# Kernel optimization log

Measured on AMD Instinct MI355X. Metric: run time of the kernel, lower is better.

## Reference

```python
import jax, jax.numpy as jnp
import numpy as np

N_HEADS = 16
ROPE_BASE = 10000.0

def rotate_half(x):
    x1, x2 = jnp.split(x, 2, axis=-1)
    return jnp.concatenate([-x2, x1], axis=-1)

def rope_tables(T, D, dtype):
    inv_freq = 1.0 / (ROPE_BASE ** (np.arange(0, D, 2, dtype=np.float32) / D))
    t = np.arange(T, dtype=np.float32)
    freqs = np.outer(t, inv_freq)            # [T, D/2]
    emb = np.concatenate([freqs, freqs], -1)  # [T, D]
    return jnp.asarray(np.cos(emb), dtype), jnp.asarray(np.sin(emb), dtype)

def setup_inputs() -> dict:
    key = jax.random.key(0)
    ks = jax.random.split(key, 5)
    B, T, C, D = 2, 2048, 1024, 64
    s = 0.02
    return {
        "x":  jax.random.normal(ks[0], (B, T, C), jnp.float32),
        "Wq": jax.random.normal(ks[1], (C, C), jnp.float32) * s,
        "Wk": jax.random.normal(ks[2], (C, D), jnp.float32) * s,
        "Wv": jax.random.normal(ks[3], (C, D), jnp.float32) * s,
        "Wo": jax.random.normal(ks[4], (C, C), jnp.float32) * s,
    }

def reference(x, Wq, Wk, Wv, Wo):
    B, T, C = x.shape
    H = N_HEADS
    D = C // H
    scale = D ** -0.5
    q = (x @ Wq).reshape(B, T, H, D).transpose(0, 2, 1, 3)  # [B,H,T,D]
    k = x @ Wk                                              # [B,T,D] single KV head
    v = x @ Wv                                              # [B,T,D]
    cos, sin = rope_tables(T, D, x.dtype)                   # [T,D]
    q = q * cos + rotate_half(q) * sin                      # broadcast over B,H
    k = k * cos + rotate_half(k) * sin                      # broadcast over B
    # MQA causal attention: shared K/V head broadcast to all query heads
    scores = jnp.einsum('bhqd,bkd->bhqk', q, k) * scale     # [B,H,T,T]
    causal = jnp.tril(jnp.ones((T, T), bool))
    scores = jnp.where(causal, scores, jnp.finfo(scores.dtype).min)
    attn = jax.nn.softmax(scores, axis=-1)
    out = jnp.einsum('bhqk,bkd->bhqd', attn, v)             # [B,H,T,D]
    out = out.transpose(0, 2, 1, 3).reshape(B, T, C)
    return out @ Wo
```

## Files before the change

kernel.cpp:

```cpp
#include <hip/hip_runtime.h>
#include <hip/hip_bf16.h>

typedef _Float16 f16;
typedef __attribute__((ext_vector_type(8))) _Float16 f16x8;
typedef __attribute__((ext_vector_type(4))) _Float16 f16x4;
typedef __attribute__((ext_vector_type(4))) float f32x4;

#define MFMA16(a, b, c) __builtin_amdgcn_mfma_f32_16x16x32_f16(a, b, c, 0, 0, 0)

__device__ __forceinline__ void gload_lds16(const void* g, void* l)
{
    __builtin_amdgcn_global_load_lds(
        (const __attribute__((address_space(1))) unsigned int*)g,
        (__attribute__((address_space(3))) unsigned int*)l, 16, 0, 0);
}

__global__ __launch_bounds__(256) void cvt_all_kernel(const float* __restrict__ x, const float* __restrict__ Wq,
                                                      const float* __restrict__ Wk, const float* __restrict__ Wv,
                                                      const float* __restrict__ Wo, f16* __restrict__ xb,
                                                      f16* __restrict__ WallT, f16* __restrict__ WoT)
{
    int i = blockIdx.x * 256 + threadIdx.x;
    if (i < 1048576) {
        float4 v = ((const float4*)x)[i];
        f16x4 o;
        o[0] = (f16)v.x; o[1] = (f16)v.y; o[2] = (f16)v.z; o[3] = (f16)v.w;
        *(f16x4*)(xb + 4 * (size_t)i) = o;
        return;
    }
    const float* src;
    f16* dstbase;
    int n4, k4, ldN;
    if (i < 1114112) {
        int j = i - 1048576;
        n4 = (j & 255) * 4; k4 = (j >> 8) * 4;
        src = Wq; ldN = 1024; dstbase = WallT + (size_t)n4 * 1024;
    } else if (i < 1122304) {
        int j = i - 1114112;
        int p4 = (j & 31) * 4; k4 = (j >> 5) * 4;
        if (p4 < 64) {
            n4 = (p4 >= 16 && p4 < 48) ? (p4 ^ 48) : p4;
            src = Wk;
        } else {
            n4 = p4 - 64;
            src = Wv;
        }
        ldN = 64; dstbase = WallT + (size_t)(1024 + p4) * 1024;
    } else {
        int j = i - 1122304;
        n4 = (j & 255) * 4; k4 = (j >> 8) * 4;
        src = Wo; ldN = 1024; dstbase = WoT + (size_t)n4 * 1024;
    }
    float4 v0 = *(const float4*)(src + (size_t)(k4 + 0) * ldN + n4);
    float4 v1 = *(const float4*)(src + (size_t)(k4 + 1) * ldN + n4);
    float4 v2 = *(const float4*)(src + (size_t)(k4 + 2) * ldN + n4);
    float4 v3 = *(const float4*)(src + (size_t)(k4 + 3) * ldN + n4);
    float a0[4] = {v0.x, v0.y, v0.z, v0.w};
    float a1[4] = {v1.x, v1.y, v1.z, v1.w};
    float a2[4] = {v2.x, v2.y, v2.z, v2.w};
    float a3[4] = {v3.x, v3.y, v3.z, v3.w};
#pragma unroll
    for (int jj = 0; jj < 4; ++jj) {
        f16x4 o;
        o[0] = (f16)a0[jj]; o[1] = (f16)a1[jj]; o[2] = (f16)a2[jj]; o[3] = (f16)a3[jj];
        *(f16x4*)(dstbase + (size_t)jj * 1024 + k4) = o;
    }
}

template<int MODE>
__global__ __launch_bounds__(256) void gemm_bt(const f16* __restrict__ A, const f16* __restrict__ Bt,
                                               void* __restrict__ Cv, f16* __restrict__ kout, f16* __restrict__ vout,
                                               int NBX)
{
    __shared__ __align__(16) f16 As[128 * 64];
    __shared__ __align__(16) f16 Bs[64 * 64];
    int id = blockIdx.x;
    int qn = gridDim.x >> 3;
    int lin = (id & 7) * qn + (id >> 3);
    int bx = lin % NBX, by = lin / NBX;
    int tid = threadIdx.x, lane = tid & 63, wid = tid >> 6;
    int wr = wid >> 1, wc = wid & 1;
    int lrow = lane & 15, gq = lane >> 4;
    f32x4 acc[4][2];
#pragma unroll
    for (int fm = 0; fm < 4; ++fm)
#pragma unroll
        for (int fn = 0; fn < 2; ++fn) acc[fm][fn] = (f32x4){0.f, 0.f, 0.f, 0.f};

    for (int kt = 0; kt < 16; ++kt) {
        int k0 = kt * 64;
#pragma unroll
        for (int i = 0; i < 4; ++i) {
            int c = wid * 4 + i;
            int row = c * 8 + (lane >> 3);
            int slot = (lane & 7) ^ (row & 7);
            gload_lds16(A + (size_t)(by * 128 + row) * 1024 + k0 + slot * 8, &As[c * 512 + lane * 8]);
        }
#pragma unroll
        for (int i = 0; i < 2; ++i) {
            int c = wid * 2 + i;
            int row = c * 8 + (lane >> 3);
            int slot = (lane & 7) ^ (row & 7);
            gload_lds16(Bt + (size_t)(bx * 64 + row) * 1024 + k0 + slot * 8, &Bs[c * 512 + lane * 8]);
        }
        __syncthreads();
#pragma unroll
        for (int ks = 0; ks < 2; ++ks) {
            f16x8 af[4], bf[2];
#pragma unroll
            for (int fm = 0; fm < 4; ++fm) {
                int row = wr * 64 + fm * 16 + lrow;
                int slot = (ks * 4 + gq) ^ (row & 7);
                af[fm] = *(const f16x8*)&As[row * 64 + slot * 8];
            }
#pragma unroll
            for (int fn = 0; fn < 2; ++fn) {
                int row = wc * 32 + fn * 16 + lrow;
                int slot = (ks * 4 + gq) ^ (row & 7);
                bf[fn] = *(const f16x8*)&Bs[row * 64 + slot * 8];
            }
#pragma unroll
            for (int fm = 0; fm < 4; ++fm)
#pragma unroll
                for (int fn = 0; fn < 2; ++fn)
                    acc[fm][fn] = MFMA16(af[fm], bf[fn], acc[fm][fn]);
        }
        __syncthreads();
    }
    if constexpr (MODE == 1) {
        float* C = (float*)Cv;
#pragma unroll
        for (int fm = 0; fm < 4; ++fm)
#pragma unroll
            for (int fn = 0; fn < 2; ++fn)
#pragma unroll
                for (int r = 0; r < 4; ++r) {
                    int row = by * 128 + wr * 64 + fm * 16 + gq * 4 + r;
                    int col = bx * 64 + wc * 32 + fn * 16 + lrow;
                    C[(size_t)row * 1024 + col] = acc[fm][fn][r];
                }
    } else {
        if (bx < 16) {
            f16* C = (f16*)Cv;
#pragma unroll
            for (int fm = 0; fm < 4; ++fm)
#pragma unroll
                for (int fn = 0; fn < 2; ++fn)
#pragma unroll
                    for (int r = 0; r < 4; ++r) {
                        int row = by * 128 + wr * 64 + fm * 16 + gq * 4 + r;
                        int col = bx * 64 + wc * 32 + fn * 16 + lrow;
                        C[(size_t)row * 1024 + col] = (f16)acc[fm][fn][r];
                    }
        } else if (bx == 16) {
            const float L2B = 13.287712379549449f / 64.0f;
            int i = wc * 16 + lrow;
            float invf = exp2f(-(float)(2 * i) * L2B);
#pragma unroll
            for (int fm = 0; fm < 4; ++fm)
#pragma unroll
                for (int r = 0; r < 4; ++r) {
                    int row = by * 128 + wr * 64 + fm * 16 + gq * 4 + r;
                    float t = (float)(row & 2047);
                    float ss, cc;
                    sincosf(t * invf, &ss, &cc);
                    float x1 = acc[fm][0][r], x2 = acc[fm][1][r];
                    kout[(size_t)row * 64 + i]      = (f16)(x1 * cc - x2 * ss);
                    kout[(size_t)row * 64 + i + 32] = (f16)(x2 * cc + x1 * ss);
                }
        } else {
#pragma unroll
            for (int fm = 0; fm < 4; ++fm)
#pragma unroll
                for (int fn = 0; fn < 2; ++fn) {
                    int d = wc * 32 + fn * 16 + lrow;
                    int rowbase = by * 128 + wr * 64 + fm * 16 + gq * 4;
                    f16x4 pw;
#pragma unroll
                    for (int r = 0; r < 4; ++r) pw[r] = (f16)acc[fm][fn][r];
                    *(f16x4*)&vout[(size_t)d * 4096 + rowbase] = pw;
                }
        }
    }
}

#define SOFTMAX(S, MM, LL, OO, PSF) do {                                            \
    float mx = fmaxf(fmaxf(fmaxf(S[0][0],S[0][1]),fmaxf(S[0][2],S[0][3])),          \
                     fmaxf(fmaxf(S[1][0],S[1][1]),fmaxf(S[1][2],S[1][3])));         \
    mx = fmaxf(mx, fmaxf(fmaxf(fmaxf(S[2][0],S[2][1]),fmaxf(S[2][2],S[2][3])),      \
                         fmaxf(fmaxf(S[3][0],S[3][1]),fmaxf(S[3][2],S[3][3]))));    \
    mx = fmaxf(mx, __shfl_xor(mx, 16));                                             \
    mx = fmaxf(mx, __shfl_xor(mx, 32));                                             \
    if (!__all(mx <= MM + 3.0f)) {                                                  \
        float mn = fmaxf(MM, mx);                                                   \
        float alpha = exp2f(MM - mn);                                               \
        MM = mn; LL *= alpha;                                                       \
        float av0 = __shfl(alpha, g * 4 + 0), av1 = __shfl(alpha, g * 4 + 1);       \
        float av2 = __shfl(alpha, g * 4 + 2), av3 = __shfl(alpha, g * 4 + 3);       \
        _Pragma("unroll")                                                           \
        for (int dt = 0; dt < 4; ++dt) {                                            \
            OO[dt][0] *= av0; OO[dt][1] *= av1; OO[dt][2] *= av2; OO[dt][3] *= av3; \
        }                                                                           \
    }                                                                               \
    float rs = 0.f;                                                                 \
    _Pragma("unroll")                                                               \
    for (int tt = 0; tt < 4; ++tt) {                                                \
        f16x4 pw;                                                                   \
        _Pragma("unroll")                                                           \
        for (int r = 0; r < 4; ++r) {                                               \
            float pp = exp2f(S[tt][r] - MM); S[tt][r] = pp; pw[r] = (f16)pp;        \
        }                                                                           \
        rs += (S[tt][0] + S[tt][1]) + (S[tt][2] + S[tt][3]);                        \
        *(f16x4*)&PSF[lrow * 64 + ((tt * 16 + g * 4) ^ swl)] = pw;                  \
    }                                                                               \
    LL += rs;                                                                       \
} while (0)

__global__ __launch_bounds__(256, 3) void attn_kernel(const f16* __restrict__ q, const f16* __restrict__ k,
                                                      const f16* __restrict__ vt, f16* __restrict__ ao,
                                                      char* __restrict__ partial)
{
    constexpr int T = 2048;
    int c = blockIdx.x, y = blockIdx.y;
    int b = y >> 3, hA = y & 7, hB = hA + 8;
    int qt, ch;
    if (c < 16)      { qt = 16 + c; ch = 0; }
    else if (c < 32) { qt = c;      ch = 1; }
    else             { qt = 47 - c; ch = 0; }
    int nt = qt + 1;
    int nch = (qt >= 16) ? 2 : 1;
    int tbeg = ch * 16;
    int tend = min(nt, tbeg + 16);

    int tid = threadIdx.x, lane = tid & 63, wid = tid >> 6;
    int lrow = lane & 15, g = lane >> 4;
    int qw = qt * 64 + wid * 16;
    int swl = (lrow & 7) << 3;

    __shared__ __align__(16) f16 Ks[2][64 * 64];
    __shared__ __align__(16) f16 Vs[2][64 * 64];
    __shared__ __align__(16) f16 PsM[4][2][16 * 64];

    const f16* qrowA = q + (size_t)(b * T + qw + lrow) * 1024 + hA * 64;
    const f16* qrowB = qrowA + (hB - hA) * 64;
    f16x8 xA0 = *(const f16x8*)&qrowA[g * 8];
    f16x8 xA1 = *(const f16x8*)&qrowA[g * 8 + 32];
    f16x8 xB0 = *(const f16x8*)&qrowB[g * 8];
    f16x8 xB1 = *(const f16x8*)&qrowB[g * 8 + 32];
    f16x8 qfA0, qfA1, qfB0, qfB1;
    {
        const float qsc = 0.125f * 1.4426950408889634f;
        const float L2B = 13.287712379549449f / 64.0f;
        float t_ = (float)(qw + lrow);
#pragma unroll
        for (int j = 0; j < 8; ++j) {
            int i = g * 8 + j;
            float invf = exp2f(-(float)(2 * i) * L2B);
            float ss, cc;
            sincosf(t_ * invf, &ss, &cc);
            float a0 = (float)xA0[j], a1 = (float)xA1[j];
            qfA0[j] = (f16)((a0 * cc - a1 * ss) * qsc);
            qfA1[j] = (f16)((a1 * cc + a0 * ss) * qsc);
            float b0 = (float)xB0[j], b1 = (float)xB1[j];
            qfB0[j] = (f16)((b0 * cc - b1 * ss) * qsc);
            qfB1[j] = (f16)((b1 * cc + b0 * ss) * qsc);
        }
    }

    float mA = -1e30f, lA = 0.f, mB = -1e30f, lB = 0.f;
    f32x4 oA[4], oB[4];
#pragma unroll
    for (int dt = 0; dt < 4; ++dt) { oA[dt] = (f32x4){0.f,0.f,0.f,0.f}; oB[dt] = (f32x4){0.f,0.f,0.f,0.f}; }

    const f16* kbase = k + (size_t)b * T * 64;
    const f16* vtbase = vt + (size_t)b * T;

    int srow_lo = lane >> 3, sslot = lane & 7;
#define STAGE(buf, t) do {                                                                   \
    _Pragma("unroll")                                                                        \
    for (int i_ = 0; i_ < 2; ++i_) {                                                         \
        int c2 = wid * 2 + i_;                                                               \
        int row = c2 * 8 + srow_lo;                                                          \
        int slot = sslot ^ (row & 7);                                                        \
        gload_lds16(kbase + (size_t)((t) * 64 + row) * 64 + slot * 8,                        \
                    &Ks[buf][c2 * 512 + lane * 8]);                                          \
        gload_lds16(vtbase + (size_t)row * 4096 + (t) * 64 + slot * 8,                       \
                    &Vs[buf][c2 * 512 + lane * 8]);                                          \
    }                                                                                        \
} while (0)

    STAGE(0, tbeg);
    __syncthreads();
    int cur = 0;

    for (int t = tbeg; t < tend; ++t) {
        if (t + 1 < tend) STAGE(cur ^ 1, t + 1);
        f16* PsA = &PsM[wid][0][0];
        f16* PsBf = &PsM[wid][1][0];
        const f16* Kc = &Ks[cur][0];
        const f16* Vc = &Vs[cur][0];

        f32x4 sA[4], sB[4];
        __builtin_amdgcn_s_setprio(1);
#pragma unroll
        for (int tt = 0; tt < 4; ++tt) {
            f16x8 kf0 = *(const f16x8*)&Kc[(tt * 16 + lrow) * 64 + ((g * 8) ^ swl)];
            f16x8 kf1 = *(const f16x8*)&Kc[(tt * 16 + lrow) * 64 + ((32 + g * 8) ^ swl)];
            f32x4 z = (f32x4){0.f, 0.f, 0.f, 0.f};
            z = MFMA16(kf0, qfA0, z);
            z = MFMA16(kf1, qfA1, z);
            sA[tt] = z;
            z = (f32x4){0.f, 0.f, 0.f, 0.f};
            z = MFMA16(kf0, qfB0, z);
            z = MFMA16(kf1, qfB1, z);
            sB[tt] = z;
        }
        __builtin_amdgcn_s_setprio(0);
        if (t == nt - 1) {
            int qab = qw + lrow;
            int kb0 = t * 64 + g * 4;
#pragma unroll
            for (int tt = 0; tt < 4; ++tt)
#pragma unroll
                for (int r = 0; r < 4; ++r)
                    if (kb0 + tt * 16 + r > qab) { sA[tt][r] = -1e30f; sB[tt][r] = -1e30f; }
        }
        SOFTMAX(sA, mA, lA, oA, PsA);
        SOFTMAX(sB, mB, lB, oB, PsBf);
        __builtin_amdgcn_s_setprio(1);
#pragma unroll
        for (int chk = 0; chk < 2; ++chk) {
            f16x8 pfA = *(const f16x8*)&PsA[lrow * 64 + ((chk * 32 + g * 8) ^ swl)];
            f16x8 pfB = *(const f16x8*)&PsBf[lrow * 64 + ((chk * 32 + g * 8) ^ swl)];
#pragma unroll
            for (int dt = 0; dt < 4; ++dt) {
                f16x8 vf = *(const f16x8*)&Vc[(dt * 16 + lrow) * 64 + ((chk * 32 + g * 8) ^ swl)];
                oA[dt] = MFMA16(pfA, vf, oA[dt]);
                oB[dt] = MFMA16(pfB, vf, oB[dt]);
            }
        }
        __builtin_amdgcn_s_setprio(0);
        __syncthreads();
        cur ^= 1;
    }
#undef STAGE
    lA += __shfl_xor(lA, 16); lA += __shfl_xor(lA, 32);
    lB += __shfl_xor(lB, 16); lB += __shfl_xor(lB, 32);

    if (nch == 1) {
#pragma unroll
        for (int rr = 0; rr < 4; ++rr) {
            float invA = 1.f / __shfl(lA, g * 4 + rr);
            float invB = 1.f / __shfl(lB, g * 4 + rr);
            int qab = qw + g * 4 + rr;
            size_t rowoff = (size_t)(b * T + qab) * 1024;
#pragma unroll
            for (int dt = 0; dt < 4; ++dt) {
                ao[rowoff + hA * 64 + dt * 16 + lrow] = (f16)(oA[dt][rr] * invA);
                ao[rowoff + hB * 64 + dt * 16 + lrow] = (f16)(oB[dt][rr] * invB);
            }
        }
    } else {
        int bhA = b * 16 + hA, bhB = b * 16 + hB;
        char* slotA = partial + ((size_t)(bhA * 16 + (qt - 16)) * 2 + ch) * 8704;
        char* slotB = partial + ((size_t)(bhB * 16 + (qt - 16)) * 2 + ch) * 8704;
        f16* opA = (f16*)slotA; float* mpA = (float*)(slotA + 8192); float* lpA = mpA + 64;
        f16* opB = (f16*)slotB; float* mpB = (float*)(slotB + 8192); float* lpB = mpB + 64;
#pragma unroll
        for (int rr = 0; rr < 4; ++rr) {
            int row = wid * 16 + g * 4 + rr;
#pragma unroll
            for (int dt = 0; dt < 4; ++dt) {
                opA[row * 64 + dt * 16 + lrow] = (f16)oA[dt][rr];
                opB[row * 64 + dt * 16 + lrow] = (f16)oB[dt][rr];
            }
        }
        if (g == 0) {
            mpA[wid * 16 + lrow] = mA; lpA[wid * 16 + lrow] = lA;
            mpB[wid * 16 + lrow] = mB; lpB[wid * 16 + lrow] = lB;
        }
    }
}

__global__ __launch_bounds__(256) void combine_kernel(const char* __restrict__ partial, f16* __restrict__ ao)
{
    constexpr int T = 2048;
    int qt = 16 + blockIdx.x, bh = blockIdx.y;
    int b = bh >> 4, h = bh & 15;
    int tid = threadIdx.x;
    int row = tid >> 2, dp = (tid & 3) * 16;
    const char* s0 = partial + ((size_t)(bh * 16 + (qt - 16)) * 2) * 8704;
    const char* s1 = s0 + 8704;
    const f16* o0 = (const f16*)s0; const float* m0 = (const float*)(s0 + 8192); const float* l0 = m0 + 64;
    const f16* o1 = (const f16*)s1; const float* m1 = (const float*)(s1 + 8192); const float* l1 = m1 + 64;
    float mm0 = m0[row], mm1 = m1[row];
    float M = fmaxf(mm0, mm1);
    float a0 = exp2f(mm0 - M), a1 = exp2f(mm1 - M);
    float inv = 1.f / (l0[row] * a0 + l1[row] * a1);
    f16x8 u0 = ((const f16x8*)(o0 + row * 64 + dp))[0];
    f16x8 u1 = ((const f16x8*)(o0 + row * 64 + dp))[1];
    f16x8 w0 = ((const f16x8*)(o1 + row * 64 + dp))[0];
    f16x8 w1 = ((const f16x8*)(o1 + row * 64 + dp))[1];
    f16x8 r0, r1;
#pragma unroll
    for (int j = 0; j < 8; ++j) {
        r0[j] = (f16)(((float)u0[j] * a0 + (float)w0[j] * a1) * inv);
        r1[j] = (f16)(((float)u1[j] * a0 + (float)w1[j] * a1) * inv);
    }
    f16* dst = ao + (size_t)(b * T + qt * 64 + row) * 1024 + h * 64 + dp;
    *(f16x8*)dst = r0;
    *(f16x8*)(dst + 8) = r1;
}

extern "C" void kernel_launch(void* const* d_in, const int* in_sizes, int n_in,
                              void* d_out, int out_size, void* d_ws, size_t ws_size,
                              hipStream_t stream)
{
    (void)in_sizes; (void)n_in; (void)out_size; (void)ws_size;
    const float* x  = (const float*)d_in[0];
    const float* Wq = (const float*)d_in[1];
    const float* Wk = (const float*)d_in[2];
    const float* Wv = (const float*)d_in[3];
    const float* Wo = (const float*)d_in[4];
    float* out = (float*)d_out;

    char* w = (char*)d_ws;
    size_t off = 0;
    auto alloc = [&](size_t bytes) -> void* {
        void* p = (void*)(w + off);
        off += (bytes + 255) & ~(size_t)255;
        return p;
    };
    f16* xb    = (f16*)alloc(4194304ull * 2);
    f16* WallT = (f16*)alloc(1179648ull * 2);
    f16* WoT   = (f16*)alloc(1048576ull * 2);
    f16* qg    = (f16*)alloc(4194304ull * 2);
    f16* krp   = (f16*)alloc(262144ull * 2);
    f16* vt    = (f16*)alloc(262144ull * 2);
    f16* ao    = (f16*)alloc(4194304ull * 2);
    char* partial = (char*)xb;

    cvt_all_kernel<<<4640, 256, 0, stream>>>(x, Wq, Wk, Wv, Wo, xb, WallT, WoT);
    gemm_bt<0><<<576, 256, 0, stream>>>(xb, WallT, qg, krp, vt, 18);
    attn_kernel<<<dim3(48, 16), 256, 0, stream>>>(qg, krp, vt, ao, partial);
    combine_kernel<<<dim3(16, 32), 256, 0, stream>>>(partial, ao);
    gemm_bt<1><<<512, 256, 0, stream>>>(ao, WoT, out, nullptr, nullptr, 16);
}
```

Measured before the change: 100.2 us.

## Rebalance causal attention split-KV chunks and serialize per-head softmax to cut LDS

The attention work split changes from fixed 16-tile chunks to even splits: query tiles 0-15 use one chunk, 16-25 use two and 26-31 use three. The grid grows to 54 blocks per row, and the combine kernel now merges up to three partials using the new slot layout. The two heads' softmax and PV MFMA phases now share one P scratch buffer in sequence. This halves that LDS footprint so launch bounds can ask for 4 blocks per CU. The softmax also skips the cross-lane max shuffles unless a rescale is needed; the tradeoffs are more partial traffic and less overlap between the two heads.

```diff
diff --git a/kernel.cpp b/kernel.cpp
--- a/kernel.cpp
+++ b/kernel.cpp
@@ -185,13 +185,13 @@
 }
 
 #define SOFTMAX(S, MM, LL, OO, PSF) do {                                            \
-    float mx = fmaxf(fmaxf(fmaxf(S[0][0],S[0][1]),fmaxf(S[0][2],S[0][3])),          \
-                     fmaxf(fmaxf(S[1][0],S[1][1]),fmaxf(S[1][2],S[1][3])));         \
-    mx = fmaxf(mx, fmaxf(fmaxf(fmaxf(S[2][0],S[2][1]),fmaxf(S[2][2],S[2][3])),      \
-                         fmaxf(fmaxf(S[3][0],S[3][1]),fmaxf(S[3][2],S[3][3]))));    \
-    mx = fmaxf(mx, __shfl_xor(mx, 16));                                             \
-    mx = fmaxf(mx, __shfl_xor(mx, 32));                                             \
-    if (!__all(mx <= MM + 3.0f)) {                                                  \
+    float mxl = fmaxf(fmaxf(fmaxf(S[0][0],S[0][1]),fmaxf(S[0][2],S[0][3])),         \
+                      fmaxf(fmaxf(S[1][0],S[1][1]),fmaxf(S[1][2],S[1][3])));        \
+    mxl = fmaxf(mxl, fmaxf(fmaxf(fmaxf(S[2][0],S[2][1]),fmaxf(S[2][2],S[2][3])),    \
+                           fmaxf(fmaxf(S[3][0],S[3][1]),fmaxf(S[3][2],S[3][3]))));  \
+    if (!__all(mxl <= MM + 3.0f)) {                                                 \
+        float mx = fmaxf(mxl, __shfl_xor(mxl, 16));                                 \
+        mx = fmaxf(mx, __shfl_xor(mx, 32));                                         \
         float mn = fmaxf(MM, mx);                                                   \
         float alpha = exp2f(MM - mn);                                               \
         MM = mn; LL *= alpha;                                                       \
@@ -216,21 +216,20 @@
     LL += rs;                                                                       \
 } while (0)
 
-__global__ __launch_bounds__(256, 3) void attn_kernel(const f16* __restrict__ q, const f16* __restrict__ k,
+__global__ __launch_bounds__(256, 4) void attn_kernel(const f16* __restrict__ q, const f16* __restrict__ k,
                                                       const f16* __restrict__ vt, f16* __restrict__ ao,
                                                       char* __restrict__ partial)
 {
     constexpr int T = 2048;
     int c = blockIdx.x, y = blockIdx.y;
     int b = y >> 3, hA = y & 7, hB = hA + 8;
-    int qt, ch;
-    if (c < 16)      { qt = 16 + c; ch = 0; }
-    else if (c < 32) { qt = c;      ch = 1; }
-    else             { qt = 47 - c; ch = 0; }
+    int qt, ch, nch;
+    if (c < 16)      { qt = c; ch = 0; nch = 1; }
+    else if (c < 36) { int j = c - 16; qt = 16 + (j >> 1); ch = j & 1;  nch = 2; }
+    else             { int j = c - 36; qt = 26 + j / 3;    ch = j % 3;  nch = 3; }
     int nt = qt + 1;
-    int nch = (qt >= 16) ? 2 : 1;
-    int tbeg = ch * 16;
-    int tend = min(nt, tbeg + 16);
+    int tbeg = ch * nt / nch;
+    int tend = (ch + 1) * nt / nch;
 
     int tid = threadIdx.x, lane = tid & 63, wid = tid >> 6;
     int lrow = lane & 15, g = lane >> 4;
@@ -239,7 +238,7 @@
 
     __shared__ __align__(16) f16 Ks[2][64 * 64];
     __shared__ __align__(16) f16 Vs[2][64 * 64];
-    __shared__ __align__(16) f16 PsM[4][2][16 * 64];
+    __shared__ __align__(16) f16 PsM[4][16 * 64];
 
     const f16* qrowA = q + (size_t)(b * T + qw + lrow) * 1024 + hA * 64;
     const f16* qrowB = qrowA + (hB - hA) * 64;
@@ -295,8 +294,7 @@
 
     for (int t = tbeg; t < tend; ++t) {
         if (t + 1 < tend) STAGE(cur ^ 1, t + 1);
-        f16* PsA = &PsM[wid][0][0];
-        f16* PsBf = &PsM[wid][1][0];
+        f16* Ps = &PsM[wid][0];
         const f16* Kc = &Ks[cur][0];
         const f16* Vc = &Vs[cur][0];
 
@@ -325,18 +323,27 @@
                 for (int r = 0; r < 4; ++r)
                     if (kb0 + tt * 16 + r > qab) { sA[tt][r] = -1e30f; sB[tt][r] = -1e30f; }
         }
-        SOFTMAX(sA, mA, lA, oA, PsA);
-        SOFTMAX(sB, mB, lB, oB, PsBf);
+        SOFTMAX(sA, mA, lA, oA, Ps);
         __builtin_amdgcn_s_setprio(1);
 #pragma unroll
         for (int chk = 0; chk < 2; ++chk) {
-            f16x8 pfA = *(const f16x8*)&PsA[lrow * 64 + ((chk * 32 + g * 8) ^ swl)];
-            f16x8 pfB = *(const f16x8*)&PsBf[lrow * 64 + ((chk * 32 + g * 8) ^ swl)];
+            f16x8 pf = *(const f16x8*)&Ps[lrow * 64 + ((chk * 32 + g * 8) ^ swl)];
 #pragma unroll
             for (int dt = 0; dt < 4; ++dt) {
                 f16x8 vf = *(const f16x8*)&Vc[(dt * 16 + lrow) * 64 + ((chk * 32 + g * 8) ^ swl)];
-                oA[dt] = MFMA16(pfA, vf, oA[dt]);
-                oB[dt] = MFMA16(pfB, vf, oB[dt]);
+                oA[dt] = MFMA16(pf, vf, oA[dt]);
+            }
+        }
+        __builtin_amdgcn_s_setprio(0);
+        SOFTMAX(sB, mB, lB, oB, Ps);
+        __builtin_amdgcn_s_setprio(1);
+#pragma unroll
+        for (int chk = 0; chk < 2; ++chk) {
+            f16x8 pf = *(const f16x8*)&Ps[lrow * 64 + ((chk * 32 + g * 8) ^ swl)];
+#pragma unroll
+            for (int dt = 0; dt < 4; ++dt) {
+                f16x8 vf = *(const f16x8*)&Vc[(dt * 16 + lrow) * 64 + ((chk * 32 + g * 8) ^ swl)];
+                oB[dt] = MFMA16(pf, vf, oB[dt]);
             }
         }
         __builtin_amdgcn_s_setprio(0);
@@ -361,9 +368,10 @@
             }
         }
     } else {
+        int offq = (qt < 26) ? (qt - 16) * 2 : 20 + (qt - 26) * 3;
         int bhA = b * 16 + hA, bhB = b * 16 + hB;
-        char* slotA = partial + ((size_t)(bhA * 16 + (qt - 16)) * 2 + ch) * 8704;
-        char* slotB = partial + ((size_t)(bhB * 16 + (qt - 16)) * 2 + ch) * 8704;
+        char* slotA = partial + ((size_t)(bhA * 38 + offq + ch)) * 8704;
+        char* slotB = partial + ((size_t)(bhB * 38 + offq + ch)) * 8704;
         f16* opA = (f16*)slotA; float* mpA = (float*)(slotA + 8192); float* lpA = mpA + 64;
         f16* opB = (f16*)slotB; float* mpB = (float*)(slotB + 8192); float* lpB = mpB + 64;
 #pragma unroll
@@ -389,23 +397,49 @@
     int b = bh >> 4, h = bh & 15;
     int tid = threadIdx.x;
     int row = tid >> 2, dp = (tid & 3) * 16;
-    const char* s0 = partial + ((size_t)(bh * 16 + (qt - 16)) * 2) * 8704;
-    const char* s1 = s0 + 8704;
-    const f16* o0 = (const f16*)s0; const float* m0 = (const float*)(s0 + 8192); const float* l0 = m0 + 64;
-    const f16* o1 = (const f16*)s1; const float* m1 = (const float*)(s1 + 8192); const float* l1 = m1 + 64;
-    float mm0 = m0[row], mm1 = m1[row];
-    float M = fmaxf(mm0, mm1);
-    float a0 = exp2f(mm0 - M), a1 = exp2f(mm1 - M);
-    float inv = 1.f / (l0[row] * a0 + l1[row] * a1);
-    f16x8 u0 = ((const f16x8*)(o0 + row * 64 + dp))[0];
-    f16x8 u1 = ((const f16x8*)(o0 + row * 64 + dp))[1];
-    f16x8 w0 = ((const f16x8*)(o1 + row * 64 + dp))[0];
-    f16x8 w1 = ((const f16x8*)(o1 + row * 64 + dp))[1];
+    int nchq = (qt < 26) ? 2 : 3;
+    int offq = (qt < 26) ? (qt - 16) * 2 : 20 + (qt - 26) * 3;
+    const char* base = partial + (size_t)(bh * 38 + offq) * 8704;
+
+    float mm[3], ll[3];
+    float M = -1e30f;
+#pragma unroll 3
+    for (int i = 0; i < 3; ++i) {
+        if (i < nchq) {
+            const char* s = base + (size_t)i * 8704;
+            mm[i] = ((const float*)(s + 8192))[row];
+            ll[i] = ((const float*)(s + 8192))[64 + row];
+            M = fmaxf(M, mm[i]);
+        }
+    }
+    float denom = 0.f, aw[3];
+#pragma unroll 3
+    for (int i = 0; i < 3; ++i) {
+        if (i < nchq) {
+            aw[i] = exp2f(mm[i] - M);
+            denom += ll[i] * aw[i];
+        }
+    }
+    float inv = 1.f / denom;
+    float acc0[8] = {0,0,0,0,0,0,0,0}, acc1[8] = {0,0,0,0,0,0,0,0};
+#pragma unroll 3
+    for (int i = 0; i < 3; ++i) {
+        if (i < nchq) {
+            const f16* op = (const f16*)(base + (size_t)i * 8704) + row * 64 + dp;
+            f16x8 u0 = ((const f16x8*)op)[0];
+            f16x8 u1 = ((const f16x8*)op)[1];
+#pragma unroll
+            for (int j = 0; j < 8; ++j) {
+                acc0[j] += (float)u0[j] * aw[i];
+                acc1[j] += (float)u1[j] * aw[i];
+            }
+        }
+    }
     f16x8 r0, r1;
 #pragma unroll
     for (int j = 0; j < 8; ++j) {
-        r0[j] = (f16)(((float)u0[j] * a0 + (float)w0[j] * a1) * inv);
-        r1[j] = (f16)(((float)u1[j] * a0 + (float)w1[j] * a1) * inv);
+        r0[j] = (f16)(acc0[j] * inv);
+        r1[j] = (f16)(acc1[j] * inv);
     }
     f16* dst = ao + (size_t)(b * T + qt * 64 + row) * 1024 + h * 64 + dp;
     *(f16x8*)dst = r0;
@@ -442,7 +476,7 @@
 
     cvt_all_kernel<<<4640, 256, 0, stream>>>(x, Wq, Wk, Wv, Wo, xb, WallT, WoT);
     gemm_bt<0><<<576, 256, 0, stream>>>(xb, WallT, qg, krp, vt, 18);
-    attn_kernel<<<dim3(48, 16), 256, 0, stream>>>(qg, krp, vt, ao, partial);
+    attn_kernel<<<dim3(54, 16), 256, 0, stream>>>(qg, krp, vt, ao, partial);
     combine_kernel<<<dim3(16, 32), 256, 0, stream>>>(partial, ao);
     gemm_bt<1><<<512, 256, 0, stream>>>(ao, WoT, out, nullptr, nullptr, 16);
 }
```

After: 107.4 us. +7.2%, slower.
